# Kernel optimization log

Measured on AMD Instinct MI355X. Metric: run time of the kernel, lower is better.

The kernel has to match this reference:

```python
import jax, jax.numpy as jnp
import numpy as np

THETA = 10000.0


def rope_apply(x, pos, theta=THETA):
    # x: [..., S, d] with d even; rotates interleaved pairs (2k, 2k+1),
    # matching the block-diag 2x2 rotation matmul in the torch RoPE.
    d = x.shape[-1]
    half = d // 2
    inv_freq = 1.0 / (theta ** (2.0 * jnp.arange(half, dtype=jnp.float32) / d))
    ang = pos.astype(jnp.float32)[:, None] * inv_freq[None, :]  # [S, half]
    cos, sin = jnp.cos(ang), jnp.sin(ang)
    xe, xo = x[..., 0::2], x[..., 1::2]
    oe = cos * xe - sin * xo
    oo = sin * xe + cos * xo
    return jnp.stack([oe, oo], axis=-1).reshape(x.shape)


def setup_inputs() -> dict:
    key = jax.random.key(0)
    ks = jax.random.split(key, 5)
    B, S, D = 2, 2048, 1024
    scale = 0.02
    return {
        "x": jax.random.normal(ks[0], (B, S, D), dtype=jnp.float32),
        "token_positions": jnp.arange(S, dtype=jnp.int64 if jax.config.jax_enable_x64 else jnp.int32),
        "wq": jax.random.normal(ks[1], (D, D), dtype=jnp.float32) * scale,
        "wk": jax.random.normal(ks[2], (D, D), dtype=jnp.float32) * scale,
        "wv": jax.random.normal(ks[3], (D, D), dtype=jnp.float32) * scale,
        "wo": jax.random.normal(ks[4], (D, D), dtype=jnp.float32) * scale,
    }


def reference(x, token_positions, wq, wk, wv, wo):
    B, S, D = x.shape
    H = 16
    dk = D // H

    def split_heads(t):  # [B,S,D] -> [B,H,S,dk]
        return t.reshape(B, S, H, dk).swapaxes(1, 2)

    q = split_heads(jnp.einsum('bsd,ed->bse', x, wq))
    k = split_heads(jnp.einsum('bsd,ed->bse', x, wk))
    v = split_heads(jnp.einsum('bsd,ed->bse', x, wv))

    q = rope_apply(q, token_positions)
    k = rope_apply(k, token_positions)

    scores = jnp.einsum('bhqd,bhkd->bhqk', q, k) / jnp.sqrt(jnp.float32(dk))
    causal = jnp.tril(jnp.ones((S, S), dtype=bool))
    scores = jnp.where(causal, scores, -jnp.inf)
    p = jax.nn.softmax(scores, axis=-1)
    o = jnp.einsum('bhqk,bhkd->bhqd', p, v)          # [B,H,S,dk]
    o = o.swapaxes(1, 2).reshape(B, S, D)            # merge heads
    return jnp.einsum('bse,de->bsd', o, wo)          # out proj (wo.T)
```

## Files before the change

### kernel.cpp

```cpp
#include <hip/hip_runtime.h>

typedef unsigned short u16;
typedef __attribute__((ext_vector_type(8))) short short8;
typedef __attribute__((ext_vector_type(4))) float f32x4;

__device__ __forceinline__ u16 f2b(float f) {
  union { float f; unsigned u; } v; v.f = f;
  unsigned u = v.u;
  return (u16)((u + 0x7FFFu + ((u >> 16) & 1u)) >> 16);
}
__device__ __forceinline__ u16 f2b_trunc(float f) {
  union { float f; unsigned u; } v; v.f = f;
  return (u16)(v.u >> 16);
}
__device__ __forceinline__ void glds16(const u16* g, u16* l) {
  __builtin_amdgcn_global_load_lds((const __attribute__((address_space(1))) void*)g,
                                   (__attribute__((address_space(3))) void*)l, 16, 0, 0);
}

__global__ __launch_bounds__(256) void prep_k(const float* __restrict__ x,
                                              const float* __restrict__ wq,
                                              const float* __restrict__ wk,
                                              const float* __restrict__ wv,
                                              const float* __restrict__ wo,
                                              const int* __restrict__ pos,
                                              u16* __restrict__ xb,
                                              u16* __restrict__ wqkvb,
                                              u16* __restrict__ wob,
                                              float* __restrict__ cs) {
  int bx = blockIdx.x, tid = threadIdx.x;
  if (bx < 8192) {
    const float* src; u16* dst; int base;
    if (bx < 4096)      { src = x;  dst = xb;                base = bx; }
    else if (bx < 5120) { src = wq; dst = wqkvb;             base = bx - 4096; }
    else if (bx < 6144) { src = wk; dst = wqkvb + (1 << 20); base = bx - 5120; }
    else if (bx < 7168) { src = wv; dst = wqkvb + (2 << 20); base = bx - 6144; }
    else                { src = wo; dst = wob;               base = bx - 7168; }
    int i4 = base * 1024 + tid * 4;
    const float4 v = *(const float4*)(src + i4);
    uint2 o;
    o.x = (unsigned)f2b(v.x) | ((unsigned)f2b(v.y) << 16);
    o.y = (unsigned)f2b(v.z) | ((unsigned)f2b(v.w) << 16);
    *(uint2*)(dst + i4) = o;
  } else {
    int idx = (bx - 8192) * 256 + tid;
    int i = idx & 31, s = idx >> 5;
    float p = (float)pos[s];
    float inv = expf(-(float)i * (logf(10000.0f) / 32.0f));
    float ang = p * inv;
    cs[idx * 2]     = cosf(ang);
    cs[idx * 2 + 1] = sinf(ang);
  }
}

__global__ __launch_bounds__(128, 3) void gemm_qkv(const u16* __restrict__ A,
                                                   const u16* __restrict__ B,
                                                   const float* __restrict__ cs,
                                                   u16* __restrict__ Qr,
                                                   u16* __restrict__ Kr,
                                                   u16* __restrict__ VTg) {
  const int K = 1024;
  __shared__ u16 As[64 * 64];
  __shared__ u16 Bs[128 * 64];
  const int tid = threadIdx.x;
  const int wv = tid >> 6, lane = tid & 63;
  const int quad = lane >> 4, l16 = lane & 15;
  const int m0 = blockIdx.y * 64, n0 = blockIdx.x * 128;
  const int sw = l16 & 7;

  f32x4 acc[4][4];
  for (int i = 0; i < 4; i++)
    for (int j = 0; j < 4; j++) acc[i][j] = (f32x4){0.f, 0.f, 0.f, 0.f};

  for (int kt = 0; kt < K; kt += 64) {
    __syncthreads();
#pragma unroll
    for (int p = 0; p < 4; p++) {
      int c = p * 128 + tid;
      int row = c >> 3, k8 = (c & 7) ^ (row & 7);
      glds16(A + (size_t)(m0 + row) * K + kt + k8 * 8, As + (size_t)(c & ~63) * 8);
    }
#pragma unroll
    for (int p = 0; p < 8; p++) {
      int c = p * 128 + tid;
      int row = c >> 3, k8 = (c & 7) ^ (row & 7);
      glds16(B + (size_t)(n0 + row) * K + kt + k8 * 8, Bs + (size_t)(c & ~63) * 8);
    }
    __syncthreads();
#pragma unroll
    for (int half = 0; half < 2; half++) {
      short8 af[4], bfr[4];
      const int kc = ((half * 4 + quad) ^ sw) * 8;
#pragma unroll
      for (int i = 0; i < 4; i++)
        af[i] = *(const short8*)(As + (i * 16 + l16) * 64 + kc);
#pragma unroll
      for (int j = 0; j < 4; j++)
        bfr[j] = *(const short8*)(Bs + (wv * 64 + j * 16 + l16) * 64 + kc);
#pragma unroll
      for (int i = 0; i < 4; i++)
#pragma unroll
        for (int j = 0; j < 4; j++)
          acc[i][j] = __builtin_amdgcn_mfma_f32_16x16x32_bf16(af[i], bfr[j], acc[i][j], 0, 0, 0);
    }
  }

  const int region = n0 >> 10;
  const int b = m0 >> 11;
  if (region < 2) {
    u16* dst = region ? Kr : Qr;
    const float qs = region ? 1.0f : 0.125f * 1.44269504f;
    const bool evn = (l16 & 1) == 0;
    for (int i = 0; i < 4; i++)
      for (int j = 0; j < 4; j++) {
        int col = n0 + wv * 64 + j * 16 + l16;
        int cq = col & 1023;
        int h = cq >> 6, d = cq & 63, ifr = (d >> 1) & 31;
        for (int r = 0; r < 4; r++) {
          int s = (m0 & 2047) + i * 16 + quad * 4 + r;
          float v = acc[i][j][r];
          float vp = __shfl_xor(v, 1);
          if (evn) {
            float2 c2 = *(const float2*)(cs + (s * 32 + ifr) * 2);
            float oe = (c2.x * v - c2.y * vp) * qs;
            float oo = (c2.y * v + c2.x * vp) * qs;
            unsigned pk = (unsigned)f2b(oe) | ((unsigned)f2b(oo) << 16);
            *(unsigned*)(dst + ((size_t)(b * 16 + h) * 2048 + s) * 64 + d) = pk;
          }
        }
      }
  } else {
    for (int j = 0; j < 4; j++) {
      int col = n0 + wv * 64 + j * 16 + l16;
      int cq = col & 1023;
      int h = cq >> 6, d = cq & 63;
      u16* base = VTg + ((size_t)(b * 16 + h) * 64 + d) * 2048;
      for (int i = 0; i < 4; i++) {
        int s0 = (m0 & 2047) + i * 16 + quad * 4;
        uint2 o;
        o.x = (unsigned)f2b(acc[i][j][0]) | ((unsigned)f2b(acc[i][j][1]) << 16);
        o.y = (unsigned)f2b(acc[i][j][2]) | ((unsigned)f2b(acc[i][j][3]) << 16);
        *(uint2*)(base + s0) = o;
      }
    }
  }
}

__global__ __launch_bounds__(128, 3) void gemm_bt_f32(const u16* __restrict__ A,
                                                      const u16* __restrict__ B,
                                                      float* __restrict__ C,
                                                      int M, int N, int K) {
  __shared__ u16 As[64 * 64];
  __shared__ u16 Bs[128 * 64];
  const int tid = threadIdx.x;
  const int wv = tid >> 6, lane = tid & 63;
  const int quad = lane >> 4, l16 = lane & 15;
  const int m0 = blockIdx.y * 64, n0 = blockIdx.x * 128;
  const int sw = l16 & 7;

  f32x4 acc[4][4];
  for (int i = 0; i < 4; i++)
    for (int j = 0; j < 4; j++) acc[i][j] = (f32x4){0.f, 0.f, 0.f, 0.f};

  for (int kt = 0; kt < K; kt += 64) {
    __syncthreads();
#pragma unroll
    for (int p = 0; p < 4; p++) {
      int c = p * 128 + tid;
      int row = c >> 3, k8 = (c & 7) ^ (row & 7);
      glds16(A + (size_t)(m0 + row) * K + kt + k8 * 8, As + (size_t)(c & ~63) * 8);
    }
#pragma unroll
    for (int p = 0; p < 8; p++) {
      int c = p * 128 + tid;
      int row = c >> 3, k8 = (c & 7) ^ (row & 7);
      glds16(B + (size_t)(n0 + row) * K + kt + k8 * 8, Bs + (size_t)(c & ~63) * 8);
    }
    __syncthreads();
#pragma unroll
    for (int half = 0; half < 2; half++) {
      short8 af[4], bfr[4];
      const int kc = ((half * 4 + quad) ^ sw) * 8;
#pragma unroll
      for (int i = 0; i < 4; i++)
        af[i] = *(const short8*)(As + (i * 16 + l16) * 64 + kc);
#pragma unroll
      for (int j = 0; j < 4; j++)
        bfr[j] = *(const short8*)(Bs + (wv * 64 + j * 16 + l16) * 64 + kc);
#pragma unroll
      for (int i = 0; i < 4; i++)
#pragma unroll
        for (int j = 0; j < 4; j++)
          acc[i][j] = __builtin_amdgcn_mfma_f32_16x16x32_bf16(af[i], bfr[j], acc[i][j], 0, 0, 0);
    }
  }
  for (int i = 0; i < 4; i++)
    for (int j = 0; j < 4; j++) {
      int col = n0 + wv * 64 + j * 16 + l16;
      for (int r = 0; r < 4; r++) {
        int row = m0 + i * 16 + quad * 4 + r;
        C[(size_t)row * N + col] = acc[i][j][r];
      }
    }
}

struct AttnSM {
  u16 Ks[2][8 * 512];
  u16 Vt[2][8 * 512];
  u16 Ps[2][8 * 520];
};

template <bool DIAG>
__device__ __forceinline__ void attn_tile(const u16* Ksb, const u16* Vtb, u16* Psb,
                                          short8 qa0, short8 qa1, f32x4* oacc,
                                          float* l_r, int wl, int quad, int l16) {
  const int rowbase = wl * 16 + quad * 4;
#pragma unroll
  for (int nt = 0; nt < 4; nt++) {
    f32x4 s4 = (f32x4){0.f, 0.f, 0.f, 0.f};
    short8 b0 = *(const short8*)(Ksb + quad * 512 + (nt * 16 + l16) * 8);
    short8 b1 = *(const short8*)(Ksb + (4 + quad) * 512 + (nt * 16 + l16) * 8);
    s4 = __builtin_amdgcn_mfma_f32_16x16x32_bf16(qa0, b0, s4, 0, 0, 0);
    s4 = __builtin_amdgcn_mfma_f32_16x16x32_bf16(qa1, b1, s4, 0, 0, 0);
    int col = nt * 16 + l16;
    int cp = col >> 3, co = col & 7;
#pragma unroll
    for (int r = 0; r < 4; r++) {
      float v = s4[r];
      if (DIAG && col > rowbase + r) v = -1e30f;
      float p = exp2f(v);
      l_r[r] += p;
      int row = rowbase + r;
      int A = (cp + 2 * (row >> 3)) & 7;
      Psb[A * 520 + row * 8 + co] = f2b_trunc(p);
    }
  }
  int mr = wl * 16 + l16;
  int A0 = (quad + 2 * (mr >> 3)) & 7;
  short8 pa0 = *(const short8*)(Psb + A0 * 520 + mr * 8);
  short8 pa1 = *(const short8*)(Psb + ((A0 + 4) & 7) * 520 + mr * 8);
  int sl0 = quad ^ (l16 & 7);
#pragma unroll
  for (int nt = 0; nt < 4; nt++) {
    int d = nt * 16 + l16;
    short8 vb0 = *(const short8*)(Vtb + d * 64 + sl0 * 8);
    short8 vb1 = *(const short8*)(Vtb + d * 64 + (sl0 ^ 4) * 8);
    oacc[nt] = __builtin_amdgcn_mfma_f32_16x16x32_bf16(pa0, vb0, oacc[nt], 0, 0, 0);
    oacc[nt] = __builtin_amdgcn_mfma_f32_16x16x32_bf16(pa1, vb1, oacc[nt], 0, 0, 0);
  }
}

__global__ __launch_bounds__(512, 4) void attn_k(const u16* __restrict__ Q,
                                                 const u16* __restrict__ K,
                                                 const u16* __restrict__ VT,
                                                 u16* __restrict__ O, int S) {
  __shared__ AttnSM sm;
  const int tid = threadIdx.x;
  const int wv = tid >> 6, lane = tid & 63, quad = lane >> 4, l16 = lane & 15;
  const int grp = wv >> 2, wl = wv & 3;
  const int bh = blockIdx.x, slot = blockIdx.y;
  const int qtB = 31 - slot;
  const int qtMy = grp ? qtB : slot;
  const int q0My = qtMy * 64;
  const u16* Qg = Q + (size_t)bh * S * 64;
  const u16* Kg = K + (size_t)bh * S * 64;
  const u16* Vg = VT + (size_t)bh * S * 64;
  const int vrow_off = lane >> 3;
  const int vchunk = (lane & 7) ^ (lane >> 3);

  const u16* qrow = Qg + (size_t)(q0My + wl * 16 + l16) * 64;
  short8 qa0 = *(const short8*)(qrow + quad * 8);
  short8 qa1 = *(const short8*)(qrow + 32 + quad * 8);

  f32x4 oacc[4];
  for (int j = 0; j < 4; j++) oacc[j] = (f32x4){0.f, 0.f, 0.f, 0.f};
  float l_r[4] = {0.f, 0.f, 0.f, 0.f};
  u16* Psb = &sm.Ps[grp][0];

  glds16(Kg + (size_t)lane * 64 + wv * 8, &sm.Ks[0][wv * 512]);
  glds16(Vg + (size_t)(wv * 8 + vrow_off) * S + vchunk * 8, &sm.Vt[0][wv * 512]);

  for (int kt = 0; kt <= qtB; kt++) {
    const int cur = kt & 1;
    __syncthreads();
    if (kt < qtB) {
      const int kn = (kt + 1) * 64;
      glds16(Kg + (size_t)(kn + lane) * 64 + wv * 8, &sm.Ks[cur ^ 1][wv * 512]);
      glds16(Vg + (size_t)(wv * 8 + vrow_off) * S + kn + vchunk * 8, &sm.Vt[cur ^ 1][wv * 512]);
    }
    if (kt < qtMy)
      attn_tile<false>(&sm.Ks[cur][0], &sm.Vt[cur][0], Psb, qa0, qa1, oacc, l_r, wl, quad, l16);
    else if (kt == qtMy)
      attn_tile<true>(&sm.Ks[cur][0], &sm.Vt[cur][0], Psb, qa0, qa1, oacc, l_r, wl, quad, l16);
  }

  const int b = bh >> 4, h = bh & 15;
  const bool evn = (l16 & 1) == 0;
  const int rowbase = wl * 16 + quad * 4;
#pragma unroll
  for (int r = 0; r < 4; r++) {
    l_r[r] += __shfl_xor(l_r[r], 1); l_r[r] += __shfl_xor(l_r[r], 2);
    l_r[r] += __shfl_xor(l_r[r], 4); l_r[r] += __shfl_xor(l_r[r], 8);
    l_r[r] = 1.f / l_r[r];
  }
#pragma unroll
  for (int nt = 0; nt < 4; nt++) {
    int col = nt * 16 + l16;
#pragma unroll
    for (int r = 0; r < 4; r++) {
      float v = oacc[nt][r] * l_r[r];
      float vp = __shfl_xor(v, 1);
      if (evn) {
        int s = q0My + rowbase + r;
        unsigned pk = (unsigned)f2b(v) | ((unsigned)f2b(vp) << 16);
        *(unsigned*)(O + ((size_t)(b * S + s) * 16 + h) * 64 + col) = pk;
      }
    }
  }
}

extern "C" void kernel_launch(void* const* d_in, const int* in_sizes, int n_in,
                              void* d_out, int out_size, void* d_ws, size_t ws_size,
                              hipStream_t stream) {
  const float* x  = (const float*)d_in[0];
  const int*   tp = (const int*)d_in[1];
  const float* wq = (const float*)d_in[2];
  const float* wk = (const float*)d_in[3];
  const float* wvp = (const float*)d_in[4];
  const float* wo = (const float*)d_in[5];
  float* out = (float*)d_out;

  const int S = 2048, D = 1024;
  const int BS = 2 * S;

  char* ws = (char*)d_ws;
  u16*   xb    = (u16*)(ws);
  u16*   wqkvb = (u16*)(ws + ((size_t)8 << 20));
  u16*   wob   = (u16*)(ws + ((size_t)14 << 20));
  float* cs    = (float*)(ws + ((size_t)16 << 20));
  u16*   qr    = (u16*)(ws + ((size_t)17 << 20));
  u16*   kr    = (u16*)(ws + ((size_t)25 << 20));
  u16*   vtg   = (u16*)(ws + ((size_t)33 << 20));
  u16*   ob    = (u16*)(ws + ((size_t)42 << 20));

  prep_k<<<8448, 256, 0, stream>>>(x, wq, wk, wvp, wo, tp, xb, wqkvb, wob, cs);

  dim3 g1(3 * D / 128, BS / 64);
  gemm_qkv<<<g1, 128, 0, stream>>>(xb, wqkvb, cs, qr, kr, vtg);

  dim3 ga(32, 16);
  attn_k<<<ga, 512, 0, stream>>>(qr, kr, vtg, ob, S);

  dim3 g2(D / 128, BS / 64);
  gemm_bt_f32<<<g2, 128, 0, stream>>>(ob, wob, out, BS, D, D);
}
```

Baseline: 186.1 us.

## Double-buffer QKV GEMM LDS tiles and enlarge block tile to 128x128

The QKV projection GEMM now uses a 128x128 block tile with four waves in a 2x2 layout instead of a 64x128 tile with two waves. Each wave reuses its A and B fragments across a larger output area, which cuts global traffic per FLOP. It also double-buffers the LDS tiles, issuing the async global-to-LDS loads for the next K step before computing the current one, so load latency can overlap the MFMAs. In exchange it uses more LDS per block and launches half as many blocks, and correctness depends on the single barrier per iteration making the async LDS writes visible in time.

Result: slower. 207.3 us (+11.4%).

```diff
diff --git a/kernel.cpp b/kernel.cpp
--- a/kernel.cpp
+++ b/kernel.cpp
@@ -53,50 +53,64 @@
   }
 }
 
-__global__ __launch_bounds__(128, 3) void gemm_qkv(const u16* __restrict__ A,
+__global__ __launch_bounds__(256, 2) void gemm_qkv(const u16* __restrict__ A,
                                                    const u16* __restrict__ B,
                                                    const float* __restrict__ cs,
                                                    u16* __restrict__ Qr,
                                                    u16* __restrict__ Kr,
                                                    u16* __restrict__ VTg) {
   const int K = 1024;
-  __shared__ u16 As[64 * 64];
-  __shared__ u16 Bs[128 * 64];
+  __shared__ u16 As[2][128 * 64];
+  __shared__ u16 Bs[2][128 * 64];
   const int tid = threadIdx.x;
-  const int wv = tid >> 6, lane = tid & 63;
+  const int lane = tid & 63;
+  const int wvid = tid >> 6;
+  const int wr = wvid >> 1, wc = wvid & 1;
   const int quad = lane >> 4, l16 = lane & 15;
-  const int m0 = blockIdx.y * 64, n0 = blockIdx.x * 128;
+  const int m0 = blockIdx.y * 128, n0 = blockIdx.x * 128;
   const int sw = l16 & 7;
 
   f32x4 acc[4][4];
   for (int i = 0; i < 4; i++)
     for (int j = 0; j < 4; j++) acc[i][j] = (f32x4){0.f, 0.f, 0.f, 0.f};
 
-  for (int kt = 0; kt < K; kt += 64) {
+  const int c_ = tid;
+
+#define QKV_STAGE(bufi, ktv)                                                        \
+  do {                                                                              \
+    const int kk_ = (ktv) * 64;                                                     \
+    _Pragma("unroll")                                                               \
+    for (int p = 0; p < 4; p++) {                                                   \
+      int c = p * 256 + c_;                                                         \
+      int row = c >> 3, k8 = (c & 7) ^ (row & 7);                                   \
+      glds16(A + (size_t)(m0 + row) * K + kk_ + k8 * 8,                             \
+             As[bufi] + (size_t)(c & ~63) * 8);                                     \
+    }                                                                               \
+    _Pragma("unroll")                                                               \
+    for (int p = 0; p < 4; p++) {                                                   \
+      int c = p * 256 + c_;                                                         \
+      int row = c >> 3, k8 = (c & 7) ^ (row & 7);                                   \
+      glds16(B + (size_t)(n0 + row) * K + kk_ + k8 * 8,                             \
+             Bs[bufi] + (size_t)(c & ~63) * 8);                                     \
+    }                                                                               \
+  } while (0)
+
+  QKV_STAGE(0, 0);
+
+  for (int kt = 0; kt < 16; kt++) {
+    const int cur = kt & 1;
     __syncthreads();
-#pragma unroll
-    for (int p = 0; p < 4; p++) {
-      int c = p * 128 + tid;
-      int row = c >> 3, k8 = (c & 7) ^ (row & 7);
-      glds16(A + (size_t)(m0 + row) * K + kt + k8 * 8, As + (size_t)(c & ~63) * 8);
-    }
-#pragma unroll
-    for (int p = 0; p < 8; p++) {
-      int c = p * 128 + tid;
-      int row = c >> 3, k8 = (c & 7) ^ (row & 7);
-      glds16(B + (size_t)(n0 + row) * K + kt + k8 * 8, Bs + (size_t)(c & ~63) * 8);
-    }
-    __syncthreads();
+    if (kt < 15) QKV_STAGE(cur ^ 1, kt + 1);
 #pragma unroll
     for (int half = 0; half < 2; half++) {
       short8 af[4], bfr[4];
       const int kc = ((half * 4 + quad) ^ sw) * 8;
 #pragma unroll
       for (int i = 0; i < 4; i++)
-        af[i] = *(const short8*)(As + (i * 16 + l16) * 64 + kc);
+        af[i] = *(const short8*)(As[cur] + (wr * 64 + i * 16 + l16) * 64 + kc);
 #pragma unroll
       for (int j = 0; j < 4; j++)
-        bfr[j] = *(const short8*)(Bs + (wv * 64 + j * 16 + l16) * 64 + kc);
+        bfr[j] = *(const short8*)(Bs[cur] + (wc * 64 + j * 16 + l16) * 64 + kc);
 #pragma unroll
       for (int i = 0; i < 4; i++)
 #pragma unroll
@@ -104,6 +118,7 @@
           acc[i][j] = __builtin_amdgcn_mfma_f32_16x16x32_bf16(af[i], bfr[j], acc[i][j], 0, 0, 0);
     }
   }
+#undef QKV_STAGE
 
   const int region = n0 >> 10;
   const int b = m0 >> 11;
@@ -113,11 +128,11 @@
     const bool evn = (l16 & 1) == 0;
     for (int i = 0; i < 4; i++)
       for (int j = 0; j < 4; j++) {
-        int col = n0 + wv * 64 + j * 16 + l16;
+        int col = n0 + wc * 64 + j * 16 + l16;
         int cq = col & 1023;
         int h = cq >> 6, d = cq & 63, ifr = (d >> 1) & 31;
         for (int r = 0; r < 4; r++) {
-          int s = (m0 & 2047) + i * 16 + quad * 4 + r;
+          int s = (m0 & 2047) + wr * 64 + i * 16 + quad * 4 + r;
           float v = acc[i][j][r];
           float vp = __shfl_xor(v, 1);
           if (evn) {
@@ -131,12 +146,12 @@
       }
   } else {
     for (int j = 0; j < 4; j++) {
-      int col = n0 + wv * 64 + j * 16 + l16;
+      int col = n0 + wc * 64 + j * 16 + l16;
       int cq = col & 1023;
       int h = cq >> 6, d = cq & 63;
       u16* base = VTg + ((size_t)(b * 16 + h) * 64 + d) * 2048;
       for (int i = 0; i < 4; i++) {
-        int s0 = (m0 & 2047) + i * 16 + quad * 4;
+        int s0 = (m0 & 2047) + wr * 64 + i * 16 + quad * 4;
         uint2 o;
         o.x = (unsigned)f2b(acc[i][j][0]) | ((unsigned)f2b(acc[i][j][1]) << 16);
         o.y = (unsigned)f2b(acc[i][j][2]) | ((unsigned)f2b(acc[i][j][3]) << 16);
@@ -345,8 +360,8 @@
 
   prep_k<<<8448, 256, 0, stream>>>(x, wq, wk, wvp, wo, tp, xb, wqkvb, wob, cs);
 
-  dim3 g1(3 * D / 128, BS / 64);
-  gemm_qkv<<<g1, 128, 0, stream>>>(xb, wqkvb, cs, qr, kr, vtg);
+  dim3 g1(3 * D / 128, BS / 128);
+  gemm_qkv<<<g1, 256, 0, stream>>>(xb, wqkvb, cs, qr, kr, vtg);
 
   dim3 ga(32, 16);
   attn_k<<<ga, 512, 0, stream>>>(qr, kr, vtg, ob, S);
```
